# Performance work log

Measured on AMD Instinct MI355X. Metric: run time of the kernel, lower is better.

The kernel has to match this reference:

```python
import jax, jax.numpy as jnp
import numpy as np

ALPHA = 0.2  # LeakyReLU negative slope
NEG_INF = -9e15

def leaky_relu(x):
    return jnp.where(x >= 0, x, ALPHA * x)

def setup_inputs() -> dict:
    key = jax.random.key(0)
    ks = jax.random.split(key, 7)
    B, N, D = 8, 1024, 256
    R = 12
    return {
        "h0": jax.random.normal(ks[0], (B, N, D), jnp.float32),
        "h1": jax.random.normal(ks[1], (B, N, D), jnp.float32),
        "multi_adj": jax.random.randint(ks[2], (R, B, N, N), 0, 2, jnp.int32),
        "adj": jax.random.randint(ks[3], (B, N, N), 0, 2, jnp.int32),
        "W": jax.random.normal(ks[4], (D, D), jnp.float32) * 0.05,
        "a": jax.random.normal(ks[5], (2 * D,), jnp.float32) * 0.05,
        "A_rel": jax.random.normal(ks[6], (R, 2 * D), jnp.float32) * 0.05,
    }

def reference(h0, h1, multi_adj, adj, W, a, A_rel):
    D = W.shape[1]
    Wh0 = jnp.einsum('bnd,de->bne', h0, W)  # [B,N0,D]
    Wh1 = jnp.einsum('bnd,de->bne', h1, W)  # [B,N1,D]
    # a_input @ v decomposes into outer-sum of per-node projections
    s0 = Wh0 @ a[:D]                         # [B,N0]
    s1 = Wh1 @ a[D:]                         # [B,N1]
    e = leaky_relu(s0[:, :, None] + s1[:, None, :])  # [B,N0,N1]
    attention = jnp.where(adj > 0, e, NEG_INF)
    # 12 relation score maps, fused: r0[r,b,i] + r1[r,b,j]
    r0 = jnp.einsum('bnd,rd->rbn', Wh0, A_rel[:, :D])  # [R,B,N0]
    r1 = jnp.einsum('bnd,rd->rbn', Wh1, A_rel[:, D:])  # [R,B,N1]
    e_rel = leaky_relu(r0[:, :, :, None] + r1[:, :, None, :])  # [R,B,N0,N1]
    rel_sum = jnp.where(multi_adj > 0, e_rel, 0.0).sum(axis=0)  # [B,N0,N1]
    # note: original softmax is over dim=1 (source-node axis N0)
    att = jax.nn.softmax(attention + 0.01 * rel_sum, axis=1)
    # dropout omitted (eval mode / deterministic baseline)
    h_prime = jnp.einsum('bij,bjd->bid', att, Wh1)
    return jax.nn.elu(h_prime)  # concat=True
```

## Files before the change

### kernel.cpp

```cpp
#include <hip/hip_runtime.h>
#include <hip/hip_bf16.h>
#include <hip/hip_fp16.h>

#define BB 8
#define NN 1024
#define DD 256
#define RR 12
#define BN (BB * NN)
#define ICH 8
#define CCH (NN / ICH)

typedef __attribute__((ext_vector_type(8))) short short8v;
typedef __attribute__((ext_vector_type(4))) float f32x4;
typedef __attribute__((ext_vector_type(4))) int int4v;
typedef __attribute__((ext_vector_type(2))) uint uint2v;

static __device__ __forceinline__ ushort f2bf(float f) {
  union { float f; uint u; } v; v.f = f;
  uint r = v.u + 0x7FFF + ((v.u >> 16) & 1);
  return (ushort)(r >> 16);
}
static __device__ __forceinline__ uint pack2(float a, float b) {
  return (uint)f2bf(a) | ((uint)f2bf(b) << 16);
}
static __device__ __forceinline__ float bfround(float f) {
  union { uint u; float f; } v; v.u = (uint)f2bf(f) << 16;
  return v.f;
}

__global__ __launch_bounds__(256) void k_prep(const float* __restrict__ W,
                                              const float* __restrict__ a,
                                              const float* __restrict__ A_rel,
                                              ushort* __restrict__ WTb,
                                              float* __restrict__ Vt) {
  __shared__ float Ls[64][65];
  int blk = blockIdx.x, tid = threadIdx.x;
  if (blk < 16) {
    int k0 = (blk & 3) * 64, d0 = (blk >> 2) * 64;
    int rr = tid >> 4, c = (tid & 15) * 4;
#pragma unroll
    for (int p = 0; p < 4; ++p) {
      int row = p * 16 + rr;
      float4 v = *(const float4*)&W[(k0 + row) * DD + d0 + c];
      Ls[row][c] = v.x; Ls[row][c + 1] = v.y; Ls[row][c + 2] = v.z; Ls[row][c + 3] = v.w;
    }
    __syncthreads();
    int r2 = tid >> 3, cc = (tid & 7) * 8;
#pragma unroll
    for (int p = 0; p < 2; ++p) {
      int d = p * 32 + r2;
      uint4 q;
      q.x = pack2(Ls[cc + 0][d], Ls[cc + 1][d]);
      q.y = pack2(Ls[cc + 2][d], Ls[cc + 3][d]);
      q.z = pack2(Ls[cc + 4][d], Ls[cc + 5][d]);
      q.w = pack2(Ls[cc + 6][d], Ls[cc + 7][d]);
      *(uint4*)&WTb[(d0 + d) * DD + k0 + cc] = q;
    }
  } else {
    int idx = blk - 16;
    int half = idx >= 26 ? 1 : 0;
    int c = idx - half * 26;
    if (c >= 13) return;
    int lane = tid & 63, w = tid >> 6;
    const float* X = (c == 0) ? &a[half * DD] : &A_rel[(c - 1) * 2 * DD + half * DD];
    float4 x4 = *(const float4*)&X[lane * 4];
    for (int kk = 0; kk < 64; ++kk) {
      int k = kk * 4 + w;
      float4 w4 = *(const float4*)&W[k * DD + lane * 4];
      float p = w4.x * x4.x + w4.y * x4.y + w4.z * x4.z + w4.w * x4.w;
#pragma unroll
      for (int off = 32; off; off >>= 1) p += __shfl_xor(p, off);
      if (lane == 0) Vt[(half * 13 + c) * DD + k] = p;
    }
  }
}

__global__ __launch_bounds__(256) void k_proj(const float* __restrict__ h0,
                                              const float* __restrict__ h1,
                                              const float* __restrict__ Vt,
                                              float* __restrict__ s0, float* __restrict__ s1,
                                              float* __restrict__ r0, float* __restrict__ r1) {
  int wid = (blockIdx.x * 256 + threadIdx.x) >> 6;
  int lane = threadIdx.x & 63;
  int mat = wid >> 13;
  int row = wid & (BN - 1);
  const float* h = mat ? h1 : h0;
  float4 h4 = *(const float4*)&h[(long)row * DD + lane * 4];
  float p[13];
#pragma unroll
  for (int c = 0; c < 13; ++c) {
    float4 v4 = *(const float4*)&Vt[(mat * 13 + c) * DD + lane * 4];
    p[c] = h4.x * v4.x + h4.y * v4.y + h4.z * v4.z + h4.w * v4.w;
  }
#pragma unroll
  for (int off = 32; off; off >>= 1)
#pragma unroll
    for (int c = 0; c < 13; ++c) p[c] += __shfl_xor(p[c], off);
  if (lane == 0) {
    if (mat == 0) {
      s0[row] = p[0];
      for (int c = 1; c < 13; ++c) r0[(c - 1) * BN + row] = p[c];
    } else {
      s1[row] = p[0];
      for (int c = 1; c < 13; ++c) r1[(c - 1) * BN + row] = p[c];
    }
  }
}

__global__ __launch_bounds__(256) void k_scores(const int* __restrict__ madj,
                                                const int* __restrict__ adj,
                                                const float* __restrict__ s0,
                                                const float* __restrict__ s1,
                                                const float* __restrict__ r0,
                                                const float* __restrict__ r1,
                                                ushort* __restrict__ U,
                                                float* __restrict__ lsum) {
  int b = blockIdx.x, c = blockIdx.y;
  int tid = threadIdx.x;
  int j4 = tid * 4;
  int i0 = c * ICH;
  __shared__ float s0c[ICH];
  __shared__ float r0c[RR][ICH];
  if (tid < (RR + 1) * ICH) {
    int v = tid / ICH, i = tid % ICH;
    float x = (v == 0) ? s0[b * NN + i0 + i] : r0[(v - 1) * BN + b * NN + i0 + i];
    if (v == 0) s0c[i] = x; else r0c[v - 1][i] = x;
  }
  __syncthreads();
  float4 s14 = *(const float4*)&s1[b * NN + j4];
  float rel[ICH][4] = {};
#pragma unroll 1
  for (int r = 0; r < RR; ++r) {
    float4 r1v = *(const float4*)&r1[r * BN + b * NN + j4];
#pragma unroll
    for (int i = 0; i < ICH; ++i) {
      int4v mv = __builtin_nontemporal_load(
          (const int4v*)&madj[(((long)r * BB + b) * NN + i0 + i) * NN + j4]);
      float r0v = r0c[r][i];
      float t0 = r0v + r1v.x; t0 = t0 >= 0.f ? t0 : 0.2f * t0;
      float t1 = r0v + r1v.y; t1 = t1 >= 0.f ? t1 : 0.2f * t1;
      float t2 = r0v + r1v.z; t2 = t2 >= 0.f ? t2 : 0.2f * t2;
      float t3 = r0v + r1v.w; t3 = t3 >= 0.f ? t3 : 0.2f * t3;
      if (mv.x > 0) rel[i][0] += t0;
      if (mv.y > 0) rel[i][1] += t1;
      if (mv.z > 0) rel[i][2] += t2;
      if (mv.w > 0) rel[i][3] += t3;
    }
  }
  float l0 = 0.f, l1 = 0.f, l2 = 0.f, l3 = 0.f;
#pragma unroll
  for (int i = 0; i < ICH; ++i) {
    int4v av = __builtin_nontemporal_load(
        (const int4v*)&adj[((long)b * NN + i0 + i) * NN + j4]);
    float s0v = s0c[i];
    float u0, u1, u2, u3;
    { float e = s0v + s14.x; e = e >= 0.f ? e : 0.2f * e;
      u0 = __expf((av.x > 0 ? e : -9e15f) + 0.01f * rel[i][0] - 4.0f); }
    { float e = s0v + s14.y; e = e >= 0.f ? e : 0.2f * e;
      u1 = __expf((av.y > 0 ? e : -9e15f) + 0.01f * rel[i][1] - 4.0f); }
    { float e = s0v + s14.z; e = e >= 0.f ? e : 0.2f * e;
      u2 = __expf((av.z > 0 ? e : -9e15f) + 0.01f * rel[i][2] - 4.0f); }
    { float e = s0v + s14.w; e = e >= 0.f ? e : 0.2f * e;
      u3 = __expf((av.w > 0 ? e : -9e15f) + 0.01f * rel[i][3] - 4.0f); }
    u0 = bfround(u0); u1 = bfround(u1); u2 = bfround(u2); u3 = bfround(u3);
    uint2v so;
    so.x = pack2(u0, u1);
    so.y = pack2(u2, u3);
    __builtin_nontemporal_store(so, (uint2v*)&U[((long)b * NN + i0 + i) * NN + j4]);
    l0 += u0; l1 += u1; l2 += u2; l3 += u3;
  }
  float* lp = &lsum[b * NN + j4];
  atomicAdd(lp + 0, l0);
  atomicAdd(lp + 1, l1);
  atomicAdd(lp + 2, l2);
  atomicAdd(lp + 3, l3);
}

__global__ __launch_bounds__(256) void k_mm_wh1(const float* __restrict__ h1,
                                                const ushort* __restrict__ WTb,
                                                const float* __restrict__ lsum,
                                                ushort* __restrict__ WhT) {
  __shared__ __align__(16) char smraw[24576];
  uint4* AswQ = (uint4*)smraw;
  uint4* BswQ = (uint4*)(smraw + 8192);
  typedef ushort LtRow[72];
  LtRow* Lt = (LtRow*)smraw;
  int n0 = blockIdx.x * 128, i0 = blockIdx.y * 64;
  int tid = threadIdx.x;
  int r = tid >> 3, cs = tid & 7;
  int lane = tid & 63, wid = tid >> 6;
  int wm = wid >> 1, wn = wid & 1;
  int lr = lane & 15, g = lane >> 4;
  f32x4 acc[2][4] = {};
  for (int k0 = 0; k0 < DD; k0 += 64) {
#pragma unroll
    for (int p = 0; p < 2; ++p) {
      int row = p * 32 + r;
      const float* src = h1 + (long)(i0 + row) * DD + k0 + cs * 8;
      float4 v0 = *(const float4*)src;
      float4 v1 = *(const float4*)(src + 4);
      uint4 q;
      q.x = pack2(v0.x, v0.y); q.y = pack2(v0.z, v0.w);
      q.z = pack2(v1.x, v1.y); q.w = pack2(v1.z, v1.w);
      AswQ[row * 8 + (cs ^ (row & 7))] = q;
    }
#pragma unroll
    for (int p = 0; p < 4; ++p) {
      int row = p * 32 + r;
      uint4 q = *(const uint4*)(WTb + (long)(n0 + row) * DD + k0 + cs * 8);
      BswQ[row * 8 + (cs ^ (row & 7))] = q;
    }
    __syncthreads();
#pragma unroll
    for (int ks = 0; ks < 2; ++ks) {
      short8v af[2], bfr[4];
      int slot = ks * 4 + g;
#pragma unroll
      for (int mi = 0; mi < 2; ++mi) {
        int row = wm * 32 + mi * 16 + lr;
        af[mi] = *reinterpret_cast<const short8v*>(&AswQ[row * 8 + (slot ^ (row & 7))]);
      }
#pragma unroll
      for (int ni = 0; ni < 4; ++ni) {
        int row = wn * 64 + ni * 16 + lr;
        bfr[ni] = *reinterpret_cast<const short8v*>(&BswQ[row * 8 + (slot ^ (row & 7))]);
      }
#pragma unroll
      for (int mi = 0; mi < 2; ++mi)
#pragma unroll
        for (int ni = 0; ni < 4; ++ni)
          acc[mi][ni] = __builtin_amdgcn_mfma_f32_16x16x32_bf16(af[mi], bfr[ni], acc[mi][ni], 0, 0, 0);
    }
    __syncthreads();
  }
#pragma unroll
  for (int mi = 0; mi < 2; ++mi) {
    int ib = wm * 32 + mi * 16 + g * 4;
    float4 lv = *(const float4*)&lsum[i0 + ib];
    float inv0 = 1.0f / lv.x, inv1 = 1.0f / lv.y, inv2 = 1.0f / lv.z, inv3 = 1.0f / lv.w;
#pragma unroll
    for (int ni = 0; ni < 4; ++ni) {
      int d = wn * 64 + ni * 16 + lr;
      uint2 w;
      w.x = pack2(acc[mi][ni][0] * inv0, acc[mi][ni][1] * inv1);
      w.y = pack2(acc[mi][ni][2] * inv2, acc[mi][ni][3] * inv3);
      *(uint2*)&Lt[d][ib] = w;
    }
  }
  __syncthreads();
  int b = i0 >> 10, il = i0 & 1023;
#pragma unroll
  for (int p = 0; p < 4; ++p) {
    int row = (tid >> 3) + p * 32;
    int ch = (tid & 7) * 8;
    uint4 q = *(uint4*)&Lt[row][ch];
    *(uint4*)&WhT[((long)b * DD + n0 + row) * NN + il + ch] = q;
  }
}

__global__ __launch_bounds__(256) void k_av(const ushort* __restrict__ U,
                                            const ushort* __restrict__ WhT,
                                            float* __restrict__ out) {
  __shared__ uint4 AswQ[64 * 8];
  __shared__ uint4 BswQ[128 * 8];
  int b = blockIdx.z;
  int i0 = blockIdx.y * 64;
  int n0 = blockIdx.x * 128;
  const ushort* Sb = U + (long)b * NN * NN;
  const ushort* Bb = WhT + (long)b * DD * NN;
  int tid = threadIdx.x;
  int r = tid >> 3, cs = tid & 7;
  int lane = tid & 63, wid = tid >> 6;
  int wm = wid >> 1, wn = wid & 1;
  int lr = lane & 15, g = lane >> 4;
  f32x4 acc[2][4] = {};
  for (int k0 = 0; k0 < NN; k0 += 64) {
#pragma unroll
    for (int p = 0; p < 2; ++p) {
      int row = p * 32 + r;
      AswQ[row * 8 + (cs ^ (row & 7))] =
          *(const uint4*)(Sb + (long)(i0 + row) * NN + k0 + cs * 8);
    }
#pragma unroll
    for (int p = 0; p < 4; ++p) {
      int row = p * 32 + r;
      BswQ[row * 8 + (cs ^ (row & 7))] =
          *(const uint4*)(Bb + (long)(n0 + row) * NN + k0 + cs * 8);
    }
    __syncthreads();
#pragma unroll
    for (int ks = 0; ks < 2; ++ks) {
      short8v af[2], bfr[4];
      int slot = ks * 4 + g;
#pragma unroll
      for (int mi = 0; mi < 2; ++mi) {
        int row = wm * 32 + mi * 16 + lr;
        af[mi] = *reinterpret_cast<const short8v*>(&AswQ[row * 8 + (slot ^ (row & 7))]);
      }
#pragma unroll
      for (int ni = 0; ni < 4; ++ni) {
        int row = wn * 64 + ni * 16 + lr;
        bfr[ni] = *reinterpret_cast<const short8v*>(&BswQ[row * 8 + (slot ^ (row & 7))]);
      }
#pragma unroll
      for (int mi = 0; mi < 2; ++mi)
#pragma unroll
        for (int ni = 0; ni < 4; ++ni)
          acc[mi][ni] = __builtin_amdgcn_mfma_f32_16x16x32_bf16(af[mi], bfr[ni], acc[mi][ni], 0, 0, 0);
    }
    __syncthreads();
  }
#pragma unroll
  for (int mi = 0; mi < 2; ++mi)
#pragma unroll
    for (int ni = 0; ni < 4; ++ni)
#pragma unroll
      for (int q = 0; q < 4; ++q) {
        int row = i0 + wm * 32 + mi * 16 + g * 4 + q;
        int col = n0 + wn * 64 + ni * 16 + lr;
        float x = acc[mi][ni][q];
        x = x > 0.f ? x : expm1f(x);
        out[((long)b * NN + row) * DD + col] = x;
      }
}

extern "C" void kernel_launch(void* const* d_in, const int* in_sizes, int n_in,
                              void* d_out, int out_size, void* d_ws, size_t ws_size,
                              hipStream_t stream) {
  const float* h0 = (const float*)d_in[0];
  const float* h1 = (const float*)d_in[1];
  const int* madj = (const int*)d_in[2];
  const int* adj = (const int*)d_in[3];
  const float* W = (const float*)d_in[4];
  const float* a = (const float*)d_in[5];
  const float* A_rel = (const float*)d_in[6];
  float* out = (float*)d_out;

  float* ws = (float*)d_ws;
  float* s0 = ws;
  float* s1 = s0 + BN;
  float* r0 = s1 + BN;
  float* r1 = r0 + RR * BN;
  float* lsum = r1 + RR * BN;
  float* Vt = lsum + BN;
  ushort* WTb = (ushort*)(Vt + 26 * DD);
  ushort* WhT = WTb + DD * DD;
  ushort* Uh = WhT + (size_t)BB * DD * NN;

  hipMemsetAsync(lsum, 0, BN * sizeof(float), stream);
  k_prep<<<68, 256, 0, stream>>>(W, a, A_rel, WTb, Vt);
  k_proj<<<(2 * BN) / 4, 256, 0, stream>>>(h0, h1, Vt, s0, s1, r0, r1);
  k_scores<<<dim3(BB, CCH), 256, 0, stream>>>(madj, adj, s0, s1, r0, r1, Uh, lsum);
  k_mm_wh1<<<dim3(2, BN / 64), 256, 0, stream>>>(h1, WTb, lsum, WhT);
  k_av<<<dim3(2, NN / 64, BB), 256, 0, stream>>>(Uh, WhT, out);
}
```

Measured before the change: 175.2 us.

## Fold lsum zeroing into prep, shrink k_av tiles, use cached U stores

Zeroing of lsum moves into an extra block of the prep kernel, which removes a separate memset launch. The score kernel's relation loop is unrolled by two, and the U write becomes a regular store so it may stay in cache for the following matmul. k_av switches from 64x128 to 64x64 output tiles, doubling the grid for better occupancy at the cost of more A-tile reloads.

```diff
diff --git a/kernel.cpp b/kernel.cpp
--- a/kernel.cpp
+++ b/kernel.cpp
@@ -32,7 +32,8 @@
                                               const float* __restrict__ a,
                                               const float* __restrict__ A_rel,
                                               ushort* __restrict__ WTb,
-                                              float* __restrict__ Vt) {
+                                              float* __restrict__ Vt,
+                                              float* __restrict__ lsum) {
   __shared__ float Ls[64][65];
   int blk = blockIdx.x, tid = threadIdx.x;
   if (blk < 16) {
@@ -56,6 +57,11 @@
       q.w = pack2(Ls[cc + 6][d], Ls[cc + 7][d]);
       *(uint4*)&WTb[(d0 + d) * DD + k0 + cc] = q;
     }
+  } else if (blk == 68) {
+    float4 z = make_float4(0.f, 0.f, 0.f, 0.f);
+#pragma unroll
+    for (int p = 0; p < 8; ++p)
+      *(float4*)&lsum[(p * 256 + tid) * 4] = z;
   } else {
     int idx = blk - 16;
     int half = idx >= 26 ? 1 : 0;
@@ -129,7 +135,7 @@
   __syncthreads();
   float4 s14 = *(const float4*)&s1[b * NN + j4];
   float rel[ICH][4] = {};
-#pragma unroll 1
+#pragma unroll 2
   for (int r = 0; r < RR; ++r) {
     float4 r1v = *(const float4*)&r1[r * BN + b * NN + j4];
 #pragma unroll
@@ -166,7 +172,7 @@
     uint2v so;
     so.x = pack2(u0, u1);
     so.y = pack2(u2, u3);
-    __builtin_nontemporal_store(so, (uint2v*)&U[((long)b * NN + i0 + i) * NN + j4]);
+    *(uint2v*)&U[((long)b * NN + i0 + i) * NN + j4] = so;
     l0 += u0; l1 += u1; l2 += u2; l3 += u3;
   }
   float* lp = &lsum[b * NN + j4];
@@ -262,66 +268,56 @@
                                             const ushort* __restrict__ WhT,
                                             float* __restrict__ out) {
   __shared__ uint4 AswQ[64 * 8];
-  __shared__ uint4 BswQ[128 * 8];
+  __shared__ uint4 BswQ[64 * 8];
   int b = blockIdx.z;
   int i0 = blockIdx.y * 64;
-  int n0 = blockIdx.x * 128;
+  int n0 = blockIdx.x * 64;
   const ushort* Sb = U + (long)b * NN * NN;
   const ushort* Bb = WhT + (long)b * DD * NN;
   int tid = threadIdx.x;
   int r = tid >> 3, cs = tid & 7;
   int lane = tid & 63, wid = tid >> 6;
-  int wm = wid >> 1, wn = wid & 1;
   int lr = lane & 15, g = lane >> 4;
-  f32x4 acc[2][4] = {};
+  f32x4 acc[4] = {};
   for (int k0 = 0; k0 < NN; k0 += 64) {
 #pragma unroll
     for (int p = 0; p < 2; ++p) {
       int row = p * 32 + r;
       AswQ[row * 8 + (cs ^ (row & 7))] =
           *(const uint4*)(Sb + (long)(i0 + row) * NN + k0 + cs * 8);
-    }
-#pragma unroll
-    for (int p = 0; p < 4; ++p) {
-      int row = p * 32 + r;
       BswQ[row * 8 + (cs ^ (row & 7))] =
           *(const uint4*)(Bb + (long)(n0 + row) * NN + k0 + cs * 8);
     }
     __syncthreads();
 #pragma unroll
     for (int ks = 0; ks < 2; ++ks) {
-      short8v af[2], bfr[4];
+      short8v af, bfr[4];
       int slot = ks * 4 + g;
-#pragma unroll
-      for (int mi = 0; mi < 2; ++mi) {
-        int row = wm * 32 + mi * 16 + lr;
-        af[mi] = *reinterpret_cast<const short8v*>(&AswQ[row * 8 + (slot ^ (row & 7))]);
+      {
+        int row = wid * 16 + lr;
+        af = *reinterpret_cast<const short8v*>(&AswQ[row * 8 + (slot ^ (row & 7))]);
       }
 #pragma unroll
       for (int ni = 0; ni < 4; ++ni) {
-        int row = wn * 64 + ni * 16 + lr;
+        int row = ni * 16 + lr;
         bfr[ni] = *reinterpret_cast<const short8v*>(&BswQ[row * 8 + (slot ^ (row & 7))]);
       }
 #pragma unroll
-      for (int mi = 0; mi < 2; ++mi)
-#pragma unroll
-        for (int ni = 0; ni < 4; ++ni)
-          acc[mi][ni] = __builtin_amdgcn_mfma_f32_16x16x32_bf16(af[mi], bfr[ni], acc[mi][ni], 0, 0, 0);
-    }
-    __syncthreads();
-  }
-#pragma unroll
-  for (int mi = 0; mi < 2; ++mi)
-#pragma unroll
-    for (int ni = 0; ni < 4; ++ni)
-#pragma unroll
-      for (int q = 0; q < 4; ++q) {
-        int row = i0 + wm * 32 + mi * 16 + g * 4 + q;
-        int col = n0 + wn * 64 + ni * 16 + lr;
-        float x = acc[mi][ni][q];
-        x = x > 0.f ? x : expm1f(x);
-        out[((long)b * NN + row) * DD + col] = x;
-      }
+      for (int ni = 0; ni < 4; ++ni)
+        acc[ni] = __builtin_amdgcn_mfma_f32_16x16x32_bf16(af, bfr[ni], acc[ni], 0, 0, 0);
+    }
+    __syncthreads();
+  }
+#pragma unroll
+  for (int ni = 0; ni < 4; ++ni)
+#pragma unroll
+    for (int q = 0; q < 4; ++q) {
+      int row = i0 + wid * 16 + g * 4 + q;
+      int col = n0 + ni * 16 + lr;
+      float x = acc[ni][q];
+      x = x > 0.f ? x : expm1f(x);
+      out[((long)b * NN + row) * DD + col] = x;
+    }
 }
 
 extern "C" void kernel_launch(void* const* d_in, const int* in_sizes, int n_in,
@@ -347,10 +343,9 @@
   ushort* WhT = WTb + DD * DD;
   ushort* Uh = WhT + (size_t)BB * DD * NN;
 
-  hipMemsetAsync(lsum, 0, BN * sizeof(float), stream);
-  k_prep<<<68, 256, 0, stream>>>(W, a, A_rel, WTb, Vt);
+  k_prep<<<69, 256, 0, stream>>>(W, a, A_rel, WTb, Vt, lsum);
   k_proj<<<(2 * BN) / 4, 256, 0, stream>>>(h0, h1, Vt, s0, s1, r0, r1);
   k_scores<<<dim3(BB, CCH), 256, 0, stream>>>(madj, adj, s0, s1, r0, r1, Uh, lsum);
   k_mm_wh1<<<dim3(2, BN / 64), 256, 0, stream>>>(h1, WTb, lsum, WhT);
-  k_av<<<dim3(2, NN / 64, BB), 256, 0, stream>>>(Uh, WhT, out);
-}
+  k_av<<<dim3(DD / 64, NN / 64, BB), 256, 0, stream>>>(Uh, WhT, out);
+}
```

Result: faster. 168.4 us (-3.9%).
